# Performance work log

Hardware: AMD Instinct MI355X
Metric: run time of the kernel (lower is better)

## Reference

```python
import jax, jax.numpy as jnp
import numpy as np

N, E, F_IN, HID, H, G = 50000, 800000, 128, 128, 4, 64
D = HID // H  # per-head dim = 32


def setup_inputs() -> dict:
    key = jax.random.key(0)
    ks = jax.random.split(key, 24)
    s = 0.05
    x = jax.random.normal(ks[0], (N, F_IN), dtype=jnp.float32)
    edge_index = jax.random.randint(ks[1], (2, E), 0, N, dtype=jnp.int64)
    batch = jnp.sort(jax.random.randint(ks[2], (N,), 0, G, dtype=jnp.int64))
    p = {}
    # layer 1: in F_IN -> H*D, layer 2: in HID -> H*D; each conv has q,k,v,skip linears (bias=True)
    names = ['Wq1', 'Wk1', 'Wv1', 'Ws1', 'Wq2', 'Wk2', 'Wv2', 'Ws2']
    dims = [(F_IN, HID)] * 4 + [(HID, HID)] * 4
    for i, (nm, dm) in enumerate(zip(names, dims)):
        p[nm] = jax.random.normal(ks[3 + 2 * i], dm, dtype=jnp.float32) * s
        p['b' + nm[1:]] = jax.random.normal(ks[4 + 2 * i], (dm[1],), dtype=jnp.float32) * s
    p['Wfc'] = jax.random.normal(ks[20], (HID, 1), dtype=jnp.float32) * s
    p['bfc'] = jax.random.normal(ks[21], (1,), dtype=jnp.float32) * s
    return {'x': x, 'edge_index': edge_index, 'batch': batch, **p}


def transformer_conv(x, edge_index, Wq, bq, Wk, bk, Wv, bv, Ws, bs):
    src, dst = edge_index[0], edge_index[1]  # messages flow src -> dst
    q = (x @ Wq + bq).reshape(-1, H, D)[dst]          # [E,H,D]
    k = (x @ Wk + bk).reshape(-1, H, D)[src]          # [E,H,D]
    v = (x @ Wv + bv).reshape(-1, H, D)[src]          # [E,H,D]
    logits = jnp.einsum('ehd,ehd->eh', q, k) / jnp.sqrt(jnp.float32(D))  # [E,H]
    m = jax.ops.segment_max(logits, dst, num_segments=N)                 # [N,H]
    e = jnp.exp(logits - m[dst])
    s = jax.ops.segment_sum(e, dst, num_segments=N)                      # [N,H]
    alpha = e / s[dst]
    agg = jax.ops.segment_sum(alpha[..., None] * v, dst, num_segments=N)  # [N,H,D]
    return agg.reshape(-1, HID) + (x @ Ws + bs)


def reference(x, edge_index, batch, Wq1, bq1, Wk1, bk1, Wv1, bv1, Ws1, bs1,
              Wq2, bq2, Wk2, bk2, Wv2, bv2, Ws2, bs2, Wfc, bfc):
    h = jax.nn.relu(transformer_conv(x, edge_index, Wq1, bq1, Wk1, bk1, Wv1, bv1, Ws1, bs1))
    h = jax.nn.relu(transformer_conv(h, edge_index, Wq2, bq2, Wk2, bk2, Wv2, bv2, Ws2, bs2))
    sums = jax.ops.segment_sum(h, batch, num_segments=G)                 # [G,HID]
    cnt = jax.ops.segment_sum(jnp.ones((h.shape[0],), h.dtype), batch, num_segments=G)
    pooled = sums / jnp.maximum(cnt, 1.0)[:, None]
    return (pooled @ Wfc + bfc).squeeze(-1)
```

## Files before the change

### kernel.cpp

```cpp
#include <hip/hip_runtime.h>
#include <hip/hip_bf16.h>
#include <math.h>

#define HID 128

typedef __attribute__((ext_vector_type(8))) short short8;
typedef __attribute__((ext_vector_type(4))) short short4v;
typedef __attribute__((ext_vector_type(4))) float f32x4;
typedef __attribute__((ext_vector_type(4))) int int4v;
typedef __attribute__((ext_vector_type(4))) unsigned int uint4v;
typedef __attribute__((ext_vector_type(4))) unsigned short ushort4v;
typedef __attribute__((ext_vector_type(2))) unsigned short ushort2v;
typedef __attribute__((ext_vector_type(2))) _Float16 half2v;

static inline size_t align256(size_t x){ return (x + 255) & ~(size_t)255; }

__device__ inline float bf2f(unsigned short h) {
  union { unsigned u; float f; } uf; uf.u = ((unsigned)h) << 16; return uf.f;
}
__device__ inline unsigned short f2bf(float f) {
  union { float f; unsigned u; } uf; uf.f = f;
  unsigned r = uf.u + 0x7fff + ((uf.u >> 16) & 1);
  return (unsigned short)(r >> 16);
}
__device__ inline unsigned short f2h(float f) {
  union { _Float16 h; unsigned short u; } c; c.h = (_Float16)f; return c.u;
}
__device__ inline half2v b2h2(unsigned u) {
  union { unsigned u; half2v h; } c; c.u = u; return c.h;
}

__device__ inline float dpp_rsum8(float x) {
  int v;
  v = __builtin_amdgcn_update_dpp(0, __float_as_int(x), 0xB1, 0xF, 0xF, true);
  x += __int_as_float(v);
  v = __builtin_amdgcn_update_dpp(0, __float_as_int(x), 0x4E, 0xF, 0xF, true);
  x += __int_as_float(v);
  v = __builtin_amdgcn_update_dpp(0, __float_as_int(x), 0x141, 0xF, 0xF, true);
  x += __int_as_float(v);
  return x;
}

__global__ __launch_bounds__(512) void k_prep(
    const float* W0, const float* W1, const float* W2, const float* W3,
    const float* W4, const float* W5, const float* W6, const float* W7,
    const float* b0, const float* b1, const float* b2, const float* b3,
    const float* b4, const float* b5, const float* b6, const float* b7,
    unsigned short* Wcat, float* Bcat,
    const int* __restrict__ edst, int* __restrict__ deg, int* __restrict__ rank, int e)
{
  __shared__ float tl[32][33];
  int t = threadIdx.x;
  if (blockIdx.x >= 128) {
    for (int i = (blockIdx.x - 128) * 512 + t; i < e; i += 512 * 512)
      rank[i] = atomicAdd(&deg[edst[i]], 1);
    return;
  }
  const float* Ws[8] = {W0, W1, W2, W3, W4, W5, W6, W7};
  const float* bs[8] = {b0, b1, b2, b3, b4, b5, b6, b7};
  int m = blockIdx.x >> 4, tile = blockIdx.x & 15;
  int tr = (tile >> 2) * 32, tc = (tile & 3) * 32;
  int tx = t & 31, ty = t >> 5;
  const float* Wm = Ws[m];
  #pragma unroll
  for (int r = 0; r < 32; r += 16) tl[ty + r][tx] = Wm[(tr + ty + r) * 128 + tc + tx];
  __syncthreads();
  #pragma unroll
  for (int r = 0; r < 32; r += 16)
    Wcat[m * 16384 + (tc + ty + r) * 128 + tr + tx] = f2bf(tl[tx][ty + r]);
  if (tile == 0 && t < 128) Bcat[m * 128 + t] = bs[m][t];
}

__global__ void k_scan_a(const int* __restrict__ deg, int* __restrict__ rowptr,
                         int* __restrict__ bsum, int n) {
  __shared__ int tmp[512];
  int t = threadIdx.x, i = blockIdx.x * 512 + t;
  int v = (i < n) ? deg[i] : 0;
  tmp[t] = v;
  __syncthreads();
  for (int off = 1; off < 512; off <<= 1) {
    int u = (t >= off) ? tmp[t - off] : 0;
    __syncthreads();
    tmp[t] += u;
    __syncthreads();
  }
  if (i < n) rowptr[i] = tmp[t] - v;
  if (t == 511) bsum[blockIdx.x] = tmp[t];
}

__global__ void k_scan_c(int* __restrict__ rowptr, const int* __restrict__ bsum,
                         int n, int e, int nb) {
  __shared__ int sred[8];
  __shared__ int base_sh;
  int t = threadIdx.x;
  int v = (t < nb && t < (int)blockIdx.x) ? bsum[t] : 0;
  #pragma unroll
  for (int off = 32; off >= 1; off >>= 1) v += __shfl_xor(v, off);
  if ((t & 63) == 0) sred[t >> 6] = v;
  __syncthreads();
  if (t == 0) {
    int b = 0;
    #pragma unroll
    for (int j = 0; j < 8; ++j) b += sred[j];
    base_sh = b;
  }
  __syncthreads();
  int i = blockIdx.x * 512 + t;
  if (i < n) rowptr[i] += base_sh;
  if (i == 0) rowptr[n] = e;
}

__global__ __launch_bounds__(256) void k_scatter(
    const int* __restrict__ esrc, const int* __restrict__ edst,
    const int* __restrict__ rowptr, const int* __restrict__ rank,
    int* __restrict__ csrc, int e)
{
  for (int i = blockIdx.x * 256 + threadIdx.x; i < e; i += gridDim.x * 256)
    csrc[rowptr[edst[i]] + rank[i]] = esrc[i] << 9;
}

template<int ABF16>
__global__ __launch_bounds__(256, 3) void k_qkvs(
    const void* __restrict__ Ain, const unsigned short* __restrict__ Wl,
    const float* __restrict__ Bl, unsigned short* __restrict__ Qb,
    unsigned short* __restrict__ KVb, unsigned short* __restrict__ Sb, int n)
{
  __shared__ unsigned short sA[64 * 128];
  __shared__ unsigned short sW[128 * 128];
  const int tid = threadIdx.x;
  const int rb = blockIdx.x * 64;
  const float QSC = 0.25503487f;

  if (ABF16) {
    const unsigned short* A = (const unsigned short*)Ain;
    #pragma unroll
    for (int it = 0; it < 4; ++it) {
      int q = tid + it * 256;
      int row = q >> 4, ch = q & 15;
      int gr = rb + row;
      short8 h = {0,0,0,0,0,0,0,0};
      if (gr < n) h = *reinterpret_cast<const short8*>(A + (size_t)gr * HID + ch * 8);
      *reinterpret_cast<short8*>(&sA[row * 128 + ((ch ^ (row & 7)) << 3)]) = h;
    }
  } else {
    const float* A = (const float*)Ain;
    #pragma unroll
    for (int it = 0; it < 8; ++it) {
      int q = tid + it * 256;
      int row = q >> 5, c4 = (q & 31) * 4;
      int gr = rb + row;
      f32x4 a = {0.f, 0.f, 0.f, 0.f};
      if (gr < n) a = *reinterpret_cast<const f32x4*>(A + (size_t)gr * HID + c4);
      short4v h;
      h.x = (short)f2bf(a.x); h.y = (short)f2bf(a.y);
      h.z = (short)f2bf(a.z); h.w = (short)f2bf(a.w);
      int eloff = row * 128 + (((c4 >> 3) ^ (row & 7)) << 3) + (c4 & 7);
      *reinterpret_cast<short4v*>(&sA[eloff]) = h;
    }
  }

  const int lane = tid & 63;
  const int wv = tid >> 6;

  auto stageW = [&](int y) {
    const unsigned short* Wy = Wl + (size_t)y * 16384;
    #pragma unroll
    for (int it = 0; it < 8; ++it) {
      int q = tid + it * 256;
      int c = q >> 4, ch = q & 15;
      short8 w = *reinterpret_cast<const short8*>(Wy + c * 128 + ch * 8);
      *reinterpret_cast<short8*>(&sW[c * 128 + ((ch ^ (c & 7)) << 3)]) = w;
    }
  };

  stageW(0);
  __syncthreads();

  short8 af[4];
  #pragma unroll
  for (int ks = 0; ks < 4; ++ks) {
    int ch = ks * 4 + (lane >> 4);
    int row = wv * 16 + (lane & 15);
    af[ks] = *reinterpret_cast<const short8*>(&sA[row * 128 + ((ch ^ (row & 7)) << 3)]);
  }

  f32x4 acc[8];
  auto compute = [&]() {
    #pragma unroll
    for (int mf = 0; mf < 8; ++mf) acc[mf] = (f32x4){0.f, 0.f, 0.f, 0.f};
    #pragma unroll
    for (int ks = 0; ks < 4; ++ks) {
      int ch = ks * 4 + (lane >> 4);
      short8 wf[8];
      #pragma unroll
      for (int mf = 0; mf < 8; ++mf) {
        int wc = mf * 16 + (lane & 15);
        wf[mf] = *reinterpret_cast<const short8*>(&sW[wc * 128 + ((ch ^ (wc & 7)) << 3)]);
      }
      #pragma unroll
      for (int mf = 0; mf < 8; ++mf)
        acc[mf] = __builtin_amdgcn_mfma_f32_16x16x32_bf16(wf[mf], af[ks], acc[mf], 0, 0, 0);
    }
  };

  const int gr = rb + wv * 16 + (lane & 15);
  const int cbase = (lane >> 4) << 2;

  compute();
  if (gr < n) {
    #pragma unroll
    for (int mf = 0; mf < 8; ++mf) {
      int c0 = mf * 16 + cbase;
      f32x4 b = *reinterpret_cast<const f32x4*>(Bl + 0 * 128 + c0);
      f32x4 v = acc[mf];
      ushort4v h;
      h.x = f2h((v.x + b.x) * QSC); h.y = f2h((v.y + b.y) * QSC);
      h.z = f2h((v.z + b.z) * QSC); h.w = f2h((v.w + b.w) * QSC);
      *reinterpret_cast<ushort4v*>(Qb + (size_t)gr * HID + c0) = h;
    }
  }

  __syncthreads();
  stageW(3);
  __syncthreads();
  compute();
  if (gr < n) {
    #pragma unroll
    for (int mf = 0; mf < 8; ++mf) {
      int c0 = mf * 16 + cbase;
      f32x4 b = *reinterpret_cast<const f32x4*>(Bl + 3 * 128 + c0);
      f32x4 v = acc[mf];
      ushort4v h;
      h.x = f2h(v.x + b.x); h.y = f2h(v.y + b.y);
      h.z = f2h(v.z + b.z); h.w = f2h(v.w + b.w);
      *reinterpret_cast<ushort4v*>(Sb + (size_t)gr * HID + c0) = h;
    }
  }

  __syncthreads();
  stageW(1);
  __syncthreads();
  compute();
  f32x4 kacc[8];
  #pragma unroll
  for (int mf = 0; mf < 8; ++mf) kacc[mf] = acc[mf];

  __syncthreads();
  stageW(2);
  __syncthreads();
  compute();
  if (gr < n) {
    #pragma unroll
    for (int mf = 0; mf < 8; ++mf) {
      int c0 = mf * 16 + cbase;
      f32x4 bk = *reinterpret_cast<const f32x4*>(Bl + 1 * 128 + c0);
      f32x4 bv = *reinterpret_cast<const f32x4*>(Bl + 2 * 128 + c0);
      f32x4 kv = kacc[mf], vv = acc[mf];
      short8 h;
      h[0] = (short)f2h(kv.x + bk.x); h[1] = (short)f2h(kv.y + bk.y);
      h[2] = (short)f2h(kv.z + bk.z); h[3] = (short)f2h(kv.w + bk.w);
      h[4] = (short)f2h(vv.x + bv.x); h[5] = (short)f2h(vv.y + bv.y);
      h[6] = (short)f2h(vv.z + bv.z); h[7] = (short)f2h(vv.w + bv.w);
      *reinterpret_cast<short8*>(KVb + (size_t)gr * 256 + 2 * c0) = h;
    }
  }
}

__global__ __launch_bounds__(256, 6) void k_attn2(
    const unsigned short* __restrict__ Qb, const unsigned short* __restrict__ KVb,
    const unsigned short* __restrict__ Sb, const int* __restrict__ rowptr,
    const int* __restrict__ csrc, unsigned short* __restrict__ Hout, int n)
{
  int wid = blockIdx.x * 4 + (threadIdx.x >> 6);
  if (wid >= n) return;
  const int lane = threadIdx.x & 63;
  const int l32 = lane & 31;
  const int half = lane >> 5;

  uint2 qu = *reinterpret_cast<const uint2*>(Qb + (size_t)wid * HID + 4 * l32);
  half2v qh0 = b2h2(qu.x), qh1 = b2h2(qu.y);

  int e0 = rowptr[wid], deg = rowptr[wid + 1] - e0;
  const int* cp = csrc + e0;
  const char* kvb = (const char*)KVb + l32 * 16;

  float m = -INFINITY, s = 0.f;
  float a0 = 0.f, a1 = 0.f, a2 = 0.f, a3 = 0.f;

  auto LDo = [&](int off) -> uint4v {
    return *reinterpret_cast<const uint4v*>(kvb + (unsigned)off);
  };
  auto logit = [&](uint4v kv) -> float {
    float d = __builtin_amdgcn_fdot2(qh1, b2h2(kv.y),
              __builtin_amdgcn_fdot2(qh0, b2h2(kv.x), 0.f, false), false);
    return dpp_rsum8(d);
  };
  auto accum = [&](float p, uint4v kv) {
    half2v v0 = b2h2(kv.z), v1 = b2h2(kv.w);
    a0 = fmaf(p, (float)v0.x, a0);
    a1 = fmaf(p, (float)v0.y, a1);
    a2 = fmaf(p, (float)v1.x, a2);
    a3 = fmaf(p, (float)v1.y, a3);
  };
  auto procB = [&](uint4v kvA, uint4v kvB) {
    float lA = logit(kvA), lB = logit(kvB);
    float qm = fmaxf(lA, lB);
    if (!__all(qm <= m + 11.5f)) {
      float nm = fmaxf(m, qm);
      float cc = __builtin_amdgcn_exp2f(m - nm);
      s *= cc; a0 *= cc; a1 *= cc; a2 *= cc; a3 *= cc; m = nm;
    }
    float pA = __builtin_amdgcn_exp2f(lA - m);
    float pB = __builtin_amdgcn_exp2f(lB - m);
    s += pA + pB;
    accum(pA, kvA);
    accum(pB, kvB);
  };
  auto proc1 = [&](int idx0) {
    int idx = idx0 + half;
    bool valid = idx < deg;
    uint4v kv = LDo(valid ? cp[idx] : 0);
    float lg = logit(kv);
    lg = valid ? lg : -INFINITY;
    if (!__all(lg <= m + 11.5f)) {
      float nm = fmaxf(m, lg);
      float cc = __builtin_amdgcn_exp2f(m - nm);
      s *= cc; a0 *= cc; a1 *= cc; a2 *= cc; a3 *= cc; m = nm;
    }
    float p = valid ? __builtin_amdgcn_exp2f(lg - m) : 0.f;
    s += p;
    accum(p, kv);
  };

  int nb = deg >> 2;
  if (nb >= 2) {
    int oA0 = cp[0 + half], oA1 = cp[2 + half];
    int oB0 = cp[4 + half], oB1 = cp[6 + half];
    uint4v A0 = LDo(oA0), A1 = LDo(oA1);
    uint4v B0 = LDo(oB0), B1 = LDo(oB1);
    for (int b = 2; b < nb; ++b) {
      int base = 4 * b;
      int n0 = cp[base + half], n1 = cp[base + 2 + half];
      uint4v N0 = LDo(n0), N1 = LDo(n1);
      procB(A0, A1);
      A0 = B0; A1 = B1;
      B0 = N0; B1 = N1;
    }
    procB(A0, A1);
    procB(B0, B1);
  } else if (nb == 1) {
    procB(LDo(cp[half]), LDo(cp[2 + half]));
  }
  int tb = nb * 4, rem = deg - tb;
  if (rem > 0) proc1(tb);
  if (rem > 2) proc1(tb + 2);

  float mo = __shfl_xor(m, 32);
  float so = __shfl_xor(s, 32);
  float b0 = __shfl_xor(a0, 32), b1 = __shfl_xor(a1, 32);
  float b2 = __shfl_xor(a2, 32), b3 = __shfl_xor(a3, 32);
  float M = fmaxf(m, mo);
  float c0 = (m  > -INFINITY) ? __builtin_amdgcn_exp2f(m  - M) : 0.f;
  float c1 = (mo > -INFINITY) ? __builtin_amdgcn_exp2f(mo - M) : 0.f;
  float st = s * c0 + so * c1;
  float inv = (st > 0.f) ? 1.f / st : 0.f;
  float r0 = (a0 * c0 + b0 * c1) * inv;
  float r1 = (a1 * c0 + b1 * c1) * inv;
  float r2 = (a2 * c0 + b2 * c1) * inv;
  float r3 = (a3 * c0 + b3 * c1) * inv;

  if (half == 0) {
    ushort4v sh = *reinterpret_cast<const ushort4v*>(Sb + (size_t)wid * HID + 4 * l32);
    half2v s0 = b2h2((unsigned)sh.x | ((unsigned)sh.y << 16));
    half2v s1 = b2h2((unsigned)sh.z | ((unsigned)sh.w << 16));
    ushort4v h;
    h.x = f2bf(fmaxf(r0 + (float)s0.x, 0.f));
    h.y = f2bf(fmaxf(r1 + (float)s0.y, 0.f));
    h.z = f2bf(fmaxf(r2 + (float)s1.x, 0.f));
    h.w = f2bf(fmaxf(r3 + (float)s1.y, 0.f));
    *reinterpret_cast<ushort4v*>(Hout + (size_t)wid * HID + 4 * l32) = h;
  }
}

__global__ __launch_bounds__(256) void k_poolfc(
    const unsigned short* __restrict__ H, const int* __restrict__ batch,
    const float* __restrict__ Wfc, const float* __restrict__ bfc,
    float* __restrict__ out, int n)
{
  int g = blockIdx.x;
  int lo = 0, hi = n;
  while (lo < hi) { int mid = (lo + hi) >> 1; if (batch[mid] < g) lo = mid + 1; else hi = mid; }
  int start = lo;
  hi = n;
  while (lo < hi) { int mid = (lo + hi) >> 1; if (batch[mid] < g + 1) lo = mid + 1; else hi = mid; }
  int end = lo;

  int t = threadIdx.x;
  int col = t & 127, rr = t >> 7;
  float a0 = 0.f, a1 = 0.f, a2 = 0.f, a3 = 0.f;
  int i = start + rr;
  for (; i + 6 < end; i += 8) {
    a0 += bf2f(H[(size_t)i * HID + col]);
    a1 += bf2f(H[(size_t)(i + 2) * HID + col]);
    a2 += bf2f(H[(size_t)(i + 4) * HID + col]);
    a3 += bf2f(H[(size_t)(i + 6) * HID + col]);
  }
  for (; i < end; i += 2) a0 += bf2f(H[(size_t)i * HID + col]);
  float v = ((a0 + a1) + (a2 + a3)) * Wfc[col];

  __shared__ float red[4];
  #pragma unroll
  for (int off = 32; off >= 1; off >>= 1) v += __shfl_xor(v, off);
  if ((t & 63) == 0) red[t >> 6] = v;
  __syncthreads();
  if (t == 0) {
    float tot = (red[0] + red[1]) + (red[2] + red[3]);
    float cnt = (float)(end - start);
    out[g] = tot / fmaxf(cnt, 1.f) + bfc[0];
  }
}

extern "C" void kernel_launch(void* const* d_in, const int* in_sizes, int n_in,
                              void* d_out, int out_size, void* d_ws, size_t ws_size,
                              hipStream_t stream)
{
  const float* x   = (const float*)d_in[0];
  const int*   ei  = (const int*)d_in[1];
  const int*   bat = (const int*)d_in[2];
  const float *Wq1 = (const float*)d_in[3],  *bq1 = (const float*)d_in[4];
  const float *Wk1 = (const float*)d_in[5],  *bk1 = (const float*)d_in[6];
  const float *Wv1 = (const float*)d_in[7],  *bv1 = (const float*)d_in[8];
  const float *Ws1 = (const float*)d_in[9],  *bs1 = (const float*)d_in[10];
  const float *Wq2 = (const float*)d_in[11], *bq2 = (const float*)d_in[12];
  const float *Wk2 = (const float*)d_in[13], *bk2 = (const float*)d_in[14];
  const float *Wv2 = (const float*)d_in[15], *bv2 = (const float*)d_in[16];
  const float *Ws2 = (const float*)d_in[17], *bs2 = (const float*)d_in[18];
  const float *Wfc = (const float*)d_in[19], *bfc = (const float*)d_in[20];
  float* out = (float*)d_out;

  const int N = in_sizes[0] / HID;
  const int E = in_sizes[1] / 2;
  const int G = 64;

  char* p = (char*)d_ws;
  auto alloc = [&](size_t bytes) -> char* { char* r = p; p += align256(bytes); return r; };
  unsigned short* Qb  = (unsigned short*)alloc((size_t)N * HID * 2);
  unsigned short* KVb = (unsigned short*)alloc((size_t)N * 256 * 2);
  unsigned short* Sb  = (unsigned short*)alloc((size_t)N * HID * 2);
  unsigned short* Hb  = (unsigned short*)alloc((size_t)N * HID * 2);
  unsigned short* H2b = (unsigned short*)alloc((size_t)N * HID * 2);
  unsigned short* Wcat = (unsigned short*)alloc((size_t)8 * 128 * 128 * 2);
  float* Bcat = (float*)alloc((size_t)8 * 128 * 4);
  int* rowptr = (int*)alloc((size_t)(N + 1) * sizeof(int));
  int* deg    = (int*)alloc((size_t)N * sizeof(int));
  int* rank   = (int*)alloc((size_t)E * sizeof(int));
  int* bsum   = (int*)alloc(4096);
  int* csrc   = (int*)alloc((size_t)E * sizeof(int));

  const int* esrc = ei;
  const int* edst = ei + E;

  hipMemsetAsync(deg, 0, (size_t)N * sizeof(int), stream);

  k_prep<<<640, 512, 0, stream>>>(
      Wq1, Wk1, Wv1, Ws1, Wq2, Wk2, Wv2, Ws2,
      bq1, bk1, bv1, bs1, bq2, bk2, bv2, bs2,
      Wcat, Bcat, edst, deg, rank, E);

  int SB = (N + 511) / 512;
  k_scan_a<<<SB, 512, 0, stream>>>(deg, rowptr, bsum, N);
  k_scan_c<<<SB, 512, 0, stream>>>(rowptr, bsum, N, E, SB);
  k_scatter<<<512, 256, 0, stream>>>(esrc, edst, rowptr, rank, csrc, E);

  int QB = (N + 63) / 64;
  k_qkvs<0><<<QB, 256, 0, stream>>>(x, Wcat, Bcat, Qb, KVb, Sb, N);
  k_attn2<<<(N + 3) / 4, 256, 0, stream>>>(Qb, KVb, Sb, rowptr, csrc, Hb, N);
  k_qkvs<1><<<QB, 256, 0, stream>>>(Hb, Wcat + 4 * 16384, Bcat + 512, Qb, KVb, Sb, N);
  k_attn2<<<(N + 3) / 4, 256, 0, stream>>>(Qb, KVb, Sb, rowptr, csrc, H2b, N);
  k_poolfc<<<G, 256, 0, stream>>>(H2b, bat, Wfc, bfc, out, N);
}
```

Measured before the change: 364.7 us.

## Split QKVS projection across grid y and give attention lanes 8 features each

The QKV/skip projection kernel now launches a second grid dimension. One half computes Q and skip, the other computes K and V, which doubles block count and halves each block's serial weight-staging and MFMA passes. The cost is that each half restages and reloads the A tile. The attention kernel now has each lane handle 8 features over a quarter of the edges instead of 4 features over half, so the logit reduction needs one fewer DPP step. The end of the kernel adds a second cross-lane softmax merge level and does more per-lane accumulation.

```diff
diff --git a/kernel.cpp b/kernel.cpp
--- a/kernel.cpp
+++ b/kernel.cpp
@@ -7,10 +7,8 @@
 typedef __attribute__((ext_vector_type(8))) short short8;
 typedef __attribute__((ext_vector_type(4))) short short4v;
 typedef __attribute__((ext_vector_type(4))) float f32x4;
-typedef __attribute__((ext_vector_type(4))) int int4v;
 typedef __attribute__((ext_vector_type(4))) unsigned int uint4v;
 typedef __attribute__((ext_vector_type(4))) unsigned short ushort4v;
-typedef __attribute__((ext_vector_type(2))) unsigned short ushort2v;
 typedef __attribute__((ext_vector_type(2))) _Float16 half2v;
 
 static inline size_t align256(size_t x){ return (x + 255) & ~(size_t)255; }
@@ -30,13 +28,11 @@
   union { unsigned u; half2v h; } c; c.u = u; return c.h;
 }
 
-__device__ inline float dpp_rsum8(float x) {
+__device__ inline float dpp_rsum4(float x) {
   int v;
   v = __builtin_amdgcn_update_dpp(0, __float_as_int(x), 0xB1, 0xF, 0xF, true);
   x += __int_as_float(v);
   v = __builtin_amdgcn_update_dpp(0, __float_as_int(x), 0x4E, 0xF, 0xF, true);
-  x += __int_as_float(v);
-  v = __builtin_amdgcn_update_dpp(0, __float_as_int(x), 0x141, 0xF, 0xF, true);
   x += __int_as_float(v);
   return x;
 }
@@ -129,6 +125,7 @@
   __shared__ unsigned short sW[128 * 128];
   const int tid = threadIdx.x;
   const int rb = blockIdx.x * 64;
+  const int y = blockIdx.y;
   const float QSC = 0.25503487f;
 
   if (ABF16) {
@@ -162,18 +159,18 @@
   const int lane = tid & 63;
   const int wv = tid >> 6;
 
-  auto stageW = [&](int y) {
-    const unsigned short* Wy = Wl + (size_t)y * 16384;
+  auto stageW = [&](int w) {
+    const unsigned short* Wy = Wl + (size_t)w * 16384;
     #pragma unroll
     for (int it = 0; it < 8; ++it) {
       int q = tid + it * 256;
       int c = q >> 4, ch = q & 15;
-      short8 w = *reinterpret_cast<const short8*>(Wy + c * 128 + ch * 8);
-      *reinterpret_cast<short8*>(&sW[c * 128 + ((ch ^ (c & 7)) << 3)]) = w;
-    }
-  };
-
-  stageW(0);
+      short8 ww = *reinterpret_cast<const short8*>(Wy + c * 128 + ch * 8);
+      *reinterpret_cast<short8*>(&sW[c * 128 + ((ch ^ (c & 7)) << 3)]) = ww;
+    }
+  };
+
+  stageW(y == 0 ? 0 : 1);
   __syncthreads();
 
   short8 af[4];
@@ -207,61 +204,55 @@
   const int cbase = (lane >> 4) << 2;
 
   compute();
-  if (gr < n) {
-    #pragma unroll
-    for (int mf = 0; mf < 8; ++mf) {
-      int c0 = mf * 16 + cbase;
-      f32x4 b = *reinterpret_cast<const f32x4*>(Bl + 0 * 128 + c0);
-      f32x4 v = acc[mf];
-      ushort4v h;
-      h.x = f2h((v.x + b.x) * QSC); h.y = f2h((v.y + b.y) * QSC);
-      h.z = f2h((v.z + b.z) * QSC); h.w = f2h((v.w + b.w) * QSC);
-      *reinterpret_cast<ushort4v*>(Qb + (size_t)gr * HID + c0) = h;
-    }
-  }
-
-  __syncthreads();
-  stageW(3);
+  f32x4 kacc[8];
+  if (y == 0) {
+    if (gr < n) {
+      #pragma unroll
+      for (int mf = 0; mf < 8; ++mf) {
+        int c0 = mf * 16 + cbase;
+        f32x4 b = *reinterpret_cast<const f32x4*>(Bl + 0 * 128 + c0);
+        f32x4 v = acc[mf];
+        ushort4v h;
+        h.x = f2h((v.x + b.x) * QSC); h.y = f2h((v.y + b.y) * QSC);
+        h.z = f2h((v.z + b.z) * QSC); h.w = f2h((v.w + b.w) * QSC);
+        *reinterpret_cast<ushort4v*>(Qb + (size_t)gr * HID + c0) = h;
+      }
+    }
+  } else {
+    #pragma unroll
+    for (int mf = 0; mf < 8; ++mf) kacc[mf] = acc[mf];
+  }
+
+  __syncthreads();
+  stageW(y == 0 ? 3 : 2);
   __syncthreads();
   compute();
   if (gr < n) {
-    #pragma unroll
-    for (int mf = 0; mf < 8; ++mf) {
-      int c0 = mf * 16 + cbase;
-      f32x4 b = *reinterpret_cast<const f32x4*>(Bl + 3 * 128 + c0);
-      f32x4 v = acc[mf];
-      ushort4v h;
-      h.x = f2h(v.x + b.x); h.y = f2h(v.y + b.y);
-      h.z = f2h(v.z + b.z); h.w = f2h(v.w + b.w);
-      *reinterpret_cast<ushort4v*>(Sb + (size_t)gr * HID + c0) = h;
-    }
-  }
-
-  __syncthreads();
-  stageW(1);
-  __syncthreads();
-  compute();
-  f32x4 kacc[8];
-  #pragma unroll
-  for (int mf = 0; mf < 8; ++mf) kacc[mf] = acc[mf];
-
-  __syncthreads();
-  stageW(2);
-  __syncthreads();
-  compute();
-  if (gr < n) {
-    #pragma unroll
-    for (int mf = 0; mf < 8; ++mf) {
-      int c0 = mf * 16 + cbase;
-      f32x4 bk = *reinterpret_cast<const f32x4*>(Bl + 1 * 128 + c0);
-      f32x4 bv = *reinterpret_cast<const f32x4*>(Bl + 2 * 128 + c0);
-      f32x4 kv = kacc[mf], vv = acc[mf];
-      short8 h;
-      h[0] = (short)f2h(kv.x + bk.x); h[1] = (short)f2h(kv.y + bk.y);
-      h[2] = (short)f2h(kv.z + bk.z); h[3] = (short)f2h(kv.w + bk.w);
-      h[4] = (short)f2h(vv.x + bv.x); h[5] = (short)f2h(vv.y + bv.y);
-      h[6] = (short)f2h(vv.z + bv.z); h[7] = (short)f2h(vv.w + bv.w);
-      *reinterpret_cast<short8*>(KVb + (size_t)gr * 256 + 2 * c0) = h;
+    if (y == 0) {
+      #pragma unroll
+      for (int mf = 0; mf < 8; ++mf) {
+        int c0 = mf * 16 + cbase;
+        f32x4 b = *reinterpret_cast<const f32x4*>(Bl + 3 * 128 + c0);
+        f32x4 v = acc[mf];
+        ushort4v h;
+        h.x = f2h(v.x + b.x); h.y = f2h(v.y + b.y);
+        h.z = f2h(v.z + b.z); h.w = f2h(v.w + b.w);
+        *reinterpret_cast<ushort4v*>(Sb + (size_t)gr * HID + c0) = h;
+      }
+    } else {
+      #pragma unroll
+      for (int mf = 0; mf < 8; ++mf) {
+        int c0 = mf * 16 + cbase;
+        f32x4 bk = *reinterpret_cast<const f32x4*>(Bl + 1 * 128 + c0);
+        f32x4 bv = *reinterpret_cast<const f32x4*>(Bl + 2 * 128 + c0);
+        f32x4 kv = kacc[mf], vv = acc[mf];
+        short8 h;
+        h[0] = (short)f2h(kv.x + bk.x); h[1] = (short)f2h(kv.y + bk.y);
+        h[2] = (short)f2h(kv.z + bk.z); h[3] = (short)f2h(kv.w + bk.w);
+        h[4] = (short)f2h(vv.x + bv.x); h[5] = (short)f2h(vv.y + bv.y);
+        h[6] = (short)f2h(vv.z + bv.z); h[7] = (short)f2h(vv.w + bv.w);
+        *reinterpret_cast<short8*>(KVb + (size_t)gr * 256 + 2 * c0) = h;
+      }
     }
   }
 }
@@ -274,74 +265,79 @@
   int wid = blockIdx.x * 4 + (threadIdx.x >> 6);
   if (wid >= n) return;
   const int lane = threadIdx.x & 63;
-  const int l32 = lane & 31;
-  const int half = lane >> 5;
-
-  uint2 qu = *reinterpret_cast<const uint2*>(Qb + (size_t)wid * HID + 4 * l32);
-  half2v qh0 = b2h2(qu.x), qh1 = b2h2(qu.y);
+  const int l16 = lane & 15;
+  const int q4 = lane >> 4;
+
+  uint4v qu = *reinterpret_cast<const uint4v*>(Qb + (size_t)wid * HID + 8 * l16);
+  half2v qh0 = b2h2(qu.x), qh1 = b2h2(qu.y), qh2 = b2h2(qu.z), qh3 = b2h2(qu.w);
 
   int e0 = rowptr[wid], deg = rowptr[wid + 1] - e0;
   const int* cp = csrc + e0;
-  const char* kvb = (const char*)KVb + l32 * 16;
+  const char* kvb = (const char*)KVb + l16 * 32;
 
   float m = -INFINITY, s = 0.f;
   float a0 = 0.f, a1 = 0.f, a2 = 0.f, a3 = 0.f;
-
-  auto LDo = [&](int off) -> uint4v {
+  float a4 = 0.f, a5 = 0.f, a6 = 0.f, a7 = 0.f;
+
+  auto LD0 = [&](int off) -> uint4v {
     return *reinterpret_cast<const uint4v*>(kvb + (unsigned)off);
   };
-  auto logit = [&](uint4v kv) -> float {
-    float d = __builtin_amdgcn_fdot2(qh1, b2h2(kv.y),
-              __builtin_amdgcn_fdot2(qh0, b2h2(kv.x), 0.f, false), false);
-    return dpp_rsum8(d);
-  };
-  auto accum = [&](float p, uint4v kv) {
-    half2v v0 = b2h2(kv.z), v1 = b2h2(kv.w);
-    a0 = fmaf(p, (float)v0.x, a0);
-    a1 = fmaf(p, (float)v0.y, a1);
-    a2 = fmaf(p, (float)v1.x, a2);
-    a3 = fmaf(p, (float)v1.y, a3);
-  };
-  auto procB = [&](uint4v kvA, uint4v kvB) {
-    float lA = logit(kvA), lB = logit(kvB);
-    float qm = fmaxf(lA, lB);
-    if (!__all(qm <= m + 11.5f)) {
-      float nm = fmaxf(m, qm);
-      float cc = __builtin_amdgcn_exp2f(m - nm);
-      s *= cc; a0 *= cc; a1 *= cc; a2 *= cc; a3 *= cc; m = nm;
-    }
-    float pA = __builtin_amdgcn_exp2f(lA - m);
-    float pB = __builtin_amdgcn_exp2f(lB - m);
-    s += pA + pB;
-    accum(pA, kvA);
-    accum(pB, kvB);
-  };
-  auto proc1 = [&](int idx0) {
-    int idx = idx0 + half;
-    bool valid = idx < deg;
-    uint4v kv = LDo(valid ? cp[idx] : 0);
-    float lg = logit(kv);
-    lg = valid ? lg : -INFINITY;
+  auto LD1 = [&](int off) -> uint4v {
+    return *reinterpret_cast<const uint4v*>(kvb + (unsigned)off + 16);
+  };
+  auto logit = [&](uint4v ka, uint4v kb) -> float {
+    float d = __builtin_amdgcn_fdot2(qh1, b2h2(ka.y),
+              __builtin_amdgcn_fdot2(qh0, b2h2(ka.x), 0.f, false), false);
+    d = __builtin_amdgcn_fdot2(qh3, b2h2(kb.y),
+        __builtin_amdgcn_fdot2(qh2, b2h2(kb.x), d, false), false);
+    return dpp_rsum4(d);
+  };
+  auto accum = [&](float p, uint4v ka, uint4v kb) {
+    half2v v0 = b2h2(ka.z), v1 = b2h2(ka.w);
+    half2v v2 = b2h2(kb.z), v3 = b2h2(kb.w);
+    a0 = fmaf(p, (float)v0.x, a0); a1 = fmaf(p, (float)v0.y, a1);
+    a2 = fmaf(p, (float)v1.x, a2); a3 = fmaf(p, (float)v1.y, a3);
+    a4 = fmaf(p, (float)v2.x, a4); a5 = fmaf(p, (float)v2.y, a5);
+    a6 = fmaf(p, (float)v3.x, a6); a7 = fmaf(p, (float)v3.y, a7);
+  };
+  auto rescale = [&](float lg) {
     if (!__all(lg <= m + 11.5f)) {
       float nm = fmaxf(m, lg);
       float cc = __builtin_amdgcn_exp2f(m - nm);
-      s *= cc; a0 *= cc; a1 *= cc; a2 *= cc; a3 *= cc; m = nm;
-    }
+      s *= cc;
+      a0 *= cc; a1 *= cc; a2 *= cc; a3 *= cc;
+      a4 *= cc; a5 *= cc; a6 *= cc; a7 *= cc;
+      m = nm;
+    }
+  };
+  auto procB = [&](uint4v ka, uint4v kb) {
+    float lg = logit(ka, kb);
+    rescale(lg);
+    float p = __builtin_amdgcn_exp2f(lg - m);
+    s += p;
+    accum(p, ka, kb);
+  };
+  auto proc1 = [&](int idx0) {
+    int idx = idx0 + q4;
+    bool valid = idx < deg;
+    int off = valid ? cp[idx] : 0;
+    uint4v ka = LD0(off), kb = LD1(off);
+    float lg = logit(ka, kb);
+    lg = valid ? lg : -INFINITY;
+    rescale(lg);
     float p = valid ? __builtin_amdgcn_exp2f(lg - m) : 0.f;
     s += p;
-    accum(p, kv);
+    accum(p, ka, kb);
   };
 
   int nb = deg >> 2;
   if (nb >= 2) {
-    int oA0 = cp[0 + half], oA1 = cp[2 + half];
-    int oB0 = cp[4 + half], oB1 = cp[6 + half];
-    uint4v A0 = LDo(oA0), A1 = LDo(oA1);
-    uint4v B0 = LDo(oB0), B1 = LDo(oB1);
+    int oA = cp[0 + q4], oB = cp[4 + q4];
+    uint4v A0 = LD0(oA), A1 = LD1(oA);
+    uint4v B0 = LD0(oB), B1 = LD1(oB);
     for (int b = 2; b < nb; ++b) {
-      int base = 4 * b;
-      int n0 = cp[base + half], n1 = cp[base + 2 + half];
-      uint4v N0 = LDo(n0), N1 = LDo(n1);
+      int oN = cp[4 * b + q4];
+      uint4v N0 = LD0(oN), N1 = LD1(oN);
       procB(A0, A1);
       A0 = B0; A1 = B1;
       B0 = N0; B1 = N1;
@@ -349,36 +345,44 @@
     procB(A0, A1);
     procB(B0, B1);
   } else if (nb == 1) {
-    procB(LDo(cp[half]), LDo(cp[2 + half]));
-  }
-  int tb = nb * 4, rem = deg - tb;
-  if (rem > 0) proc1(tb);
-  if (rem > 2) proc1(tb + 2);
-
-  float mo = __shfl_xor(m, 32);
-  float so = __shfl_xor(s, 32);
-  float b0 = __shfl_xor(a0, 32), b1 = __shfl_xor(a1, 32);
-  float b2 = __shfl_xor(a2, 32), b3 = __shfl_xor(a3, 32);
-  float M = fmaxf(m, mo);
-  float c0 = (m  > -INFINITY) ? __builtin_amdgcn_exp2f(m  - M) : 0.f;
-  float c1 = (mo > -INFINITY) ? __builtin_amdgcn_exp2f(mo - M) : 0.f;
-  float st = s * c0 + so * c1;
-  float inv = (st > 0.f) ? 1.f / st : 0.f;
-  float r0 = (a0 * c0 + b0 * c1) * inv;
-  float r1 = (a1 * c0 + b1 * c1) * inv;
-  float r2 = (a2 * c0 + b2 * c1) * inv;
-  float r3 = (a3 * c0 + b3 * c1) * inv;
-
-  if (half == 0) {
-    ushort4v sh = *reinterpret_cast<const ushort4v*>(Sb + (size_t)wid * HID + 4 * l32);
-    half2v s0 = b2h2((unsigned)sh.x | ((unsigned)sh.y << 16));
-    half2v s1 = b2h2((unsigned)sh.z | ((unsigned)sh.w << 16));
-    ushort4v h;
-    h.x = f2bf(fmaxf(r0 + (float)s0.x, 0.f));
-    h.y = f2bf(fmaxf(r1 + (float)s0.y, 0.f));
-    h.z = f2bf(fmaxf(r2 + (float)s1.x, 0.f));
-    h.w = f2bf(fmaxf(r3 + (float)s1.y, 0.f));
-    *reinterpret_cast<ushort4v*>(Hout + (size_t)wid * HID + 4 * l32) = h;
+    int o = cp[q4];
+    procB(LD0(o), LD1(o));
+  }
+  if (deg & 3) proc1(nb * 4);
+
+  #pragma unroll
+  for (int lvl = 16; lvl <= 32; lvl <<= 1) {
+    float mo = __shfl_xor(m, lvl);
+    float so = __shfl_xor(s, lvl);
+    float b0 = __shfl_xor(a0, lvl), b1 = __shfl_xor(a1, lvl);
+    float b2 = __shfl_xor(a2, lvl), b3 = __shfl_xor(a3, lvl);
+    float b4 = __shfl_xor(a4, lvl), b5 = __shfl_xor(a5, lvl);
+    float b6 = __shfl_xor(a6, lvl), b7 = __shfl_xor(a7, lvl);
+    float M = fmaxf(m, mo);
+    float c0 = (m  > -INFINITY) ? __builtin_amdgcn_exp2f(m  - M) : 0.f;
+    float c1 = (mo > -INFINITY) ? __builtin_amdgcn_exp2f(mo - M) : 0.f;
+    s = s * c0 + so * c1;
+    a0 = a0 * c0 + b0 * c1; a1 = a1 * c0 + b1 * c1;
+    a2 = a2 * c0 + b2 * c1; a3 = a3 * c0 + b3 * c1;
+    a4 = a4 * c0 + b4 * c1; a5 = a5 * c0 + b5 * c1;
+    a6 = a6 * c0 + b6 * c1; a7 = a7 * c0 + b7 * c1;
+    m = M;
+  }
+  float inv = (s > 0.f) ? 1.f / s : 0.f;
+
+  if (q4 == 0) {
+    uint4v su = *reinterpret_cast<const uint4v*>(Sb + (size_t)wid * HID + 8 * l16);
+    half2v s0 = b2h2(su.x), s1 = b2h2(su.y), s2 = b2h2(su.z), s3 = b2h2(su.w);
+    short8 h;
+    h[0] = (short)f2bf(fmaxf(fmaf(a0, inv, (float)s0.x), 0.f));
+    h[1] = (short)f2bf(fmaxf(fmaf(a1, inv, (float)s0.y), 0.f));
+    h[2] = (short)f2bf(fmaxf(fmaf(a2, inv, (float)s1.x), 0.f));
+    h[3] = (short)f2bf(fmaxf(fmaf(a3, inv, (float)s1.y), 0.f));
+    h[4] = (short)f2bf(fmaxf(fmaf(a4, inv, (float)s2.x), 0.f));
+    h[5] = (short)f2bf(fmaxf(fmaf(a5, inv, (float)s2.y), 0.f));
+    h[6] = (short)f2bf(fmaxf(fmaf(a6, inv, (float)s3.x), 0.f));
+    h[7] = (short)f2bf(fmaxf(fmaf(a7, inv, (float)s3.y), 0.f));
+    *reinterpret_cast<short8*>(Hout + (size_t)wid * HID + 8 * l16) = h;
   }
 }
 
@@ -473,9 +477,10 @@
   k_scatter<<<512, 256, 0, stream>>>(esrc, edst, rowptr, rank, csrc, E);
 
   int QB = (N + 63) / 64;
-  k_qkvs<0><<<QB, 256, 0, stream>>>(x, Wcat, Bcat, Qb, KVb, Sb, N);
+  dim3 qgrid(QB, 2);
+  k_qkvs<0><<<qgrid, 256, 0, stream>>>(x, Wcat, Bcat, Qb, KVb, Sb, N);
   k_attn2<<<(N + 3) / 4, 256, 0, stream>>>(Qb, KVb, Sb, rowptr, csrc, Hb, N);
-  k_qkvs<1><<<QB, 256, 0, stream>>>(Hb, Wcat + 4 * 16384, Bcat + 512, Qb, KVb, Sb, N);
+  k_qkvs<1><<<qgrid, 256, 0, stream>>>(Hb, Wcat + 4 * 16384, Bcat + 512, Qb, KVb, Sb, N);
   k_attn2<<<(N + 3) / 4, 256, 0, stream>>>(Qb, KVb, Sb, rowptr, csrc, H2b, N);
   k_poolfc<<<G, 256, 0, stream>>>(H2b, bat, Wfc, bfc, out, N);
 }
```

New measurement: 364.4 us. About the same (-0.1%).
